# Performance work log

Measured on AMD Instinct MI355X. Metric: run time of the kernel, lower is better.

The kernel has to match this reference:

```python
import jax, jax.numpy as jnp
import numpy as np

N_EMBD = 1024
N_HEAD = 16
HEAD_DIM = N_EMBD // N_HEAD
B, T = 2, 2048


def setup_inputs() -> dict:
    key = jax.random.key(0)
    ks = jax.random.split(key, 12)
    s = 0.02
    inp = {
        "x": jax.random.normal(ks[0], (B, T, N_EMBD), dtype=jnp.float32),
        "ln1_g": jnp.ones((N_EMBD,), jnp.float32),
        "ln1_b": jnp.zeros((N_EMBD,), jnp.float32),
        "ln2_g": jnp.ones((N_EMBD,), jnp.float32),
        "ln2_b": jnp.zeros((N_EMBD,), jnp.float32),
        "W_qkv": jax.random.normal(ks[1], (N_EMBD, 3 * N_EMBD), jnp.float32) * s,
        "b_qkv": jnp.zeros((3 * N_EMBD,), jnp.float32),
        "W_o": jax.random.normal(ks[2], (N_EMBD, N_EMBD), jnp.float32) * s,
        "b_o": jnp.zeros((N_EMBD,), jnp.float32),
        "W_fc": jax.random.normal(ks[3], (N_EMBD, 4 * N_EMBD), jnp.float32) * s,
        "b_fc": jnp.zeros((4 * N_EMBD,), jnp.float32),
        "W_proj": jax.random.normal(ks[4], (4 * N_EMBD, N_EMBD), jnp.float32) * s,
        "b_proj": jnp.zeros((N_EMBD,), jnp.float32),
    }
    return inp


def _layernorm(x, g, b, eps=1e-5):
    mu = jnp.mean(x, axis=-1, keepdims=True)
    var = jnp.var(x, axis=-1, keepdims=True)
    return (x - mu) * jax.lax.rsqrt(var + eps) * g + b


def _block(x, ln1_g, ln1_b, ln2_g, ln2_b, W_qkv, b_qkv, W_o, b_o, W_fc, b_fc, W_proj, b_proj):
    # --- attention sub-block (pre-LN) ---
    h = _layernorm(x, ln1_g, ln1_b)
    qkv = h @ W_qkv + b_qkv                     # [B,T,3E]
    q, k, v = jnp.split(qkv, 3, axis=-1)
    def split_heads(t):
        return t.reshape(B, T, N_HEAD, HEAD_DIM).transpose(0, 2, 1, 3)  # [B,H,T,D]
    q, k, v = split_heads(q), split_heads(k), split_heads(v)
    scores = jnp.einsum("bhqd,bhkd->bhqk", q, k) / (HEAD_DIM ** 0.5)
    causal = jnp.tril(jnp.ones((T, T), dtype=bool))
    scores = jnp.where(causal, scores, jnp.float32(-jnp.inf))
    probs = jax.nn.softmax(scores, axis=-1)
    attn = jnp.einsum("bhqk,bhkd->bhqd", probs, v)        # [B,H,T,D]
    attn = attn.transpose(0, 2, 1, 3).reshape(B, T, N_EMBD)
    x = x + attn @ W_o + b_o
    # --- MLP sub-block (pre-LN) ---
    h = _layernorm(x, ln2_g, ln2_b)
    h = jax.nn.gelu(h @ W_fc + b_fc, approximate=False)
    x = x + h @ W_proj + b_proj
    return x


def reference(x, ln1_g, ln1_b, ln2_g, ln2_b, W_qkv, b_qkv, W_o, b_o, W_fc, b_fc, W_proj, b_proj):
    return _block(x, ln1_g, ln1_b, ln2_g, ln2_b, W_qkv, b_qkv, W_o, b_o, W_fc, b_fc, W_proj, b_proj)
```

## Files before the change

kernel.cpp:

```cpp
#include <hip/hip_runtime.h>
#include <hip/hip_bf16.h>


#define TT 2048
#define EE 1024
#define NH 16
#define HD 64

#define AS1 __attribute__((address_space(1)))
#define AS3 __attribute__((address_space(3)))

using bf16x8 = __bf16 __attribute__((ext_vector_type(8)));
using bf16x4 = __bf16 __attribute__((ext_vector_type(4)));
using f32x4  = float __attribute__((ext_vector_type(4)));

__global__ __launch_bounds__(256) void convt_kernel(const float* __restrict__ W,
                                                    __bf16* __restrict__ WT,
                                                    int K, int N) {
    __shared__ __bf16 t[32][33];
    int n0 = blockIdx.x * 32, k0 = blockIdx.y * 32;
    int tid = threadIdx.x;
    int r = tid >> 3, c4 = (tid & 7) * 4;
    float4 v = *(const float4*)(W + (size_t)(k0 + r) * N + n0 + c4);
    t[r][c4 + 0] = (__bf16)v.x; t[r][c4 + 1] = (__bf16)v.y;
    t[r][c4 + 2] = (__bf16)v.z; t[r][c4 + 3] = (__bf16)v.w;
    __syncthreads();
    bf16x4 o;
    o[0] = t[c4 + 0][r]; o[1] = t[c4 + 1][r];
    o[2] = t[c4 + 2][r]; o[3] = t[c4 + 3][r];
    *(bf16x4*)(WT + (size_t)(n0 + r) * K + k0 + c4) = o;
}

__global__ __launch_bounds__(256) void ln_kernel(const float* __restrict__ x,
                                                 const float* __restrict__ g,
                                                 const float* __restrict__ bta,
                                                 __bf16* __restrict__ out) {
    int row = blockIdx.x;
    int tid = threadIdx.x;
    const float4 xv = *(const float4*)(x + (size_t)row * EE + tid * 4);
    float s  = xv.x + xv.y + xv.z + xv.w;
    float ss = xv.x*xv.x + xv.y*xv.y + xv.z*xv.z + xv.w*xv.w;
    __shared__ float rs[256], rss[256];
    rs[tid] = s; rss[tid] = ss;
    __syncthreads();
    for (int st = 128; st > 0; st >>= 1) {
        if (tid < st) { rs[tid] += rs[tid+st]; rss[tid] += rss[tid+st]; }
        __syncthreads();
    }
    float mean = rs[0] * (1.0f / EE);
    float var  = rss[0] * (1.0f / EE) - mean * mean;
    float rstd = rsqrtf(var + 1e-5f);
    const float4 gv = *(const float4*)(g + tid * 4);
    const float4 bv = *(const float4*)(bta + tid * 4);
    bf16x4 ov;
    ov[0] = (__bf16)((xv.x - mean) * rstd * gv.x + bv.x);
    ov[1] = (__bf16)((xv.y - mean) * rstd * gv.y + bv.y);
    ov[2] = (__bf16)((xv.z - mean) * rstd * gv.z + bv.z);
    ov[3] = (__bf16)((xv.w - mean) * rstd * gv.w + bv.w);
    *(bf16x4*)(out + (size_t)row * EE + tid * 4) = ov;
}

template<int TM, int TN, bool GELU, bool RESID, typename CT>
__global__ __launch_bounds__(256) void gemm_bt_kernel(const __bf16* __restrict__ A,
                                                      const __bf16* __restrict__ BT,
                                                      const float* __restrict__ bias,
                                                      const float* resid, CT* C,
                                                      int M, int N, int K) {
    constexpr int MT = TM / 32;
    constexpr int NT = TN / 32;
    __shared__ __align__(16) __bf16 As[TM][32];
    __shared__ __align__(16) __bf16 Bs[TN][32];
    int tid = threadIdx.x, wave = tid >> 6, lane = tid & 63;
    int quad = lane >> 4, l16 = lane & 15;
    int wm = wave >> 1, wn = wave & 1;
    int m0 = blockIdx.y * TM, n0 = blockIdx.x * TN;

    f32x4 acc[MT][NT] = {};

    int srow = wave * 16 + (lane >> 2);
    int scol = (lane & 3) * 8;

    for (int kb = 0; kb < K; kb += 32) {
#pragma unroll
        for (int p = 0; p < TM / 64; p++) {
            const __bf16* g = A + (size_t)(m0 + p * 64 + srow) * K + kb + scol;
            __builtin_amdgcn_global_load_lds((AS1 const void*)g,
                                             (AS3 void*)&As[p * 64 + wave * 16][0], 16, 0, 0);
        }
#pragma unroll
        for (int p = 0; p < TN / 64; p++) {
            const __bf16* g = BT + (size_t)(n0 + p * 64 + srow) * K + kb + scol;
            __builtin_amdgcn_global_load_lds((AS1 const void*)g,
                                             (AS3 void*)&Bs[p * 64 + wave * 16][0], 16, 0, 0);
        }
        __syncthreads();
        bf16x8 af[MT], bfr[NT];
#pragma unroll
        for (int mt = 0; mt < MT; mt++)
            af[mt] = *(const bf16x8*)(&As[wm * (MT * 16) + mt * 16 + l16][quad * 8]);
#pragma unroll
        for (int nt = 0; nt < NT; nt++)
            bfr[nt] = *(const bf16x8*)(&Bs[wn * (NT * 16) + nt * 16 + l16][quad * 8]);
#pragma unroll
        for (int mt = 0; mt < MT; mt++)
#pragma unroll
            for (int nt = 0; nt < NT; nt++)
                acc[mt][nt] = __builtin_amdgcn_mfma_f32_16x16x32_bf16(af[mt], bfr[nt],
                                                                      acc[mt][nt], 0, 0, 0);
        __syncthreads();
    }

#pragma unroll
    for (int nt = 0; nt < NT; nt++) {
        int c = n0 + wn * (NT * 16) + nt * 16 + l16;
        float bv = bias[c];
#pragma unroll
        for (int mt = 0; mt < MT; mt++) {
#pragma unroll
            for (int r = 0; r < 4; r++) {
                int row = m0 + wm * (MT * 16) + mt * 16 + quad * 4 + r;
                float v = acc[mt][nt][r] + bv;
                if (GELU)  v = 0.5f * v * (1.0f + erff(v * 0.70710678118f));
                if (RESID) v += resid[(size_t)row * N + c];
                C[(size_t)row * N + c] = (CT)v;
            }
        }
    }
}

__global__ __launch_bounds__(256) void flash_attn_kernel(const __bf16* __restrict__ qkv,
                                                         __bf16* __restrict__ out) {
    int qt = (int)gridDim.x - 1 - (int)blockIdx.x;
    int h = blockIdx.y, b = blockIdx.z;
    int tid = threadIdx.x, wave = tid >> 6, lane = tid & 63;
    int quad = lane >> 4, l16 = lane & 15;
    int q0 = qt * 64;

    __shared__ __align__(16) __bf16 Ks[64][72];
    __shared__ __align__(16) __bf16 VTs[64][72];
    __shared__ __align__(16) __bf16 Ps[4][16][72];

    size_t base = (size_t)b * TT * (3 * EE);

    int qrow = q0 + wave * 16 + l16;
    const __bf16* qp = qkv + base + (size_t)qrow * (3 * EE) + h * HD;
    bf16x8 aq0 = *(const bf16x8*)(qp + quad * 8);
    bf16x8 aq1 = *(const bf16x8*)(qp + 32 + quad * 8);

    f32x4 oacc[4] = {};
    float m_i[4], l_i[4];
#pragma unroll
    for (int r = 0; r < 4; r++) { m_i[r] = -3.0e38f; l_i[r] = 0.0f; }
    int qg_base = q0 + wave * 16 + quad * 4;

    for (int kt = 0; kt <= qt; ++kt) {
        int k0 = kt * 64;
        int v = tid;
#pragma unroll
        for (int it = 0; it < 2; ++it, v += 256) {
            int row = v >> 3, col = (v & 7) * 8;
            const __bf16* kp = qkv + base + (size_t)(k0 + row) * (3 * EE) + EE + h * HD + col;
            const __bf16* vp = qkv + base + (size_t)(k0 + row) * (3 * EE) + 2 * EE + h * HD + col;
            *(bf16x8*)(&Ks[row][col]) = *(const bf16x8*)kp;
            bf16x8 vv = *(const bf16x8*)vp;
#pragma unroll
            for (int j = 0; j < 8; j++) VTs[col + j][row] = vv[j];
        }
        __syncthreads();

        f32x4 s[4] = {};
#pragma unroll
        for (int nt = 0; nt < 4; nt++) {
            bf16x8 bk0 = *(const bf16x8*)(&Ks[nt * 16 + l16][quad * 8]);
            bf16x8 bk1 = *(const bf16x8*)(&Ks[nt * 16 + l16][32 + quad * 8]);
            s[nt] = __builtin_amdgcn_mfma_f32_16x16x32_bf16(aq0, bk0, s[nt], 0, 0, 0);
            s[nt] = __builtin_amdgcn_mfma_f32_16x16x32_bf16(aq1, bk1, s[nt], 0, 0, 0);
        }

        bool maskt = (kt == qt);
        float rmax[4];
#pragma unroll
        for (int r = 0; r < 4; r++) rmax[r] = -3.0e38f;
#pragma unroll
        for (int nt = 0; nt < 4; nt++) {
            int key = k0 + nt * 16 + l16;
#pragma unroll
            for (int r = 0; r < 4; r++) {
                float sv = s[nt][r] * 0.125f;
                if (maskt && key > qg_base + r) sv = -3.0e38f;
                s[nt][r] = sv;
                rmax[r] = fmaxf(rmax[r], sv);
            }
        }
#pragma unroll
        for (int off = 1; off < 16; off <<= 1)
#pragma unroll
            for (int r = 0; r < 4; r++) rmax[r] = fmaxf(rmax[r], __shfl_xor(rmax[r], off));

        float alpha[4], rsum[4];
#pragma unroll
        for (int r = 0; r < 4; r++) {
            float mnew = fmaxf(m_i[r], rmax[r]);
            alpha[r] = __expf(m_i[r] - mnew);
            m_i[r] = mnew;
            rsum[r] = 0.0f;
        }
#pragma unroll
        for (int nt = 0; nt < 4; nt++) {
#pragma unroll
            for (int r = 0; r < 4; r++) {
                float p = __expf(s[nt][r] - m_i[r]);
                rsum[r] += p;
                Ps[wave][quad * 4 + r][nt * 16 + l16] = (__bf16)p;
            }
        }
#pragma unroll
        for (int off = 1; off < 16; off <<= 1)
#pragma unroll
            for (int r = 0; r < 4; r++) rsum[r] += __shfl_xor(rsum[r], off);
#pragma unroll
        for (int r = 0; r < 4; r++) {
            l_i[r] = l_i[r] * alpha[r] + rsum[r];
#pragma unroll
            for (int nt = 0; nt < 4; nt++) oacc[nt][r] *= alpha[r];
        }

#pragma unroll
        for (int half = 0; half < 2; half++) {
            bf16x8 ap = *(const bf16x8*)(&Ps[wave][l16][half * 32 + quad * 8]);
#pragma unroll
            for (int nt = 0; nt < 4; nt++) {
                bf16x8 bv = *(const bf16x8*)(&VTs[nt * 16 + l16][half * 32 + quad * 8]);
                oacc[nt] = __builtin_amdgcn_mfma_f32_16x16x32_bf16(ap, bv, oacc[nt], 0, 0, 0);
            }
        }
        __syncthreads();
    }

#pragma unroll
    for (int nt = 0; nt < 4; nt++) {
#pragma unroll
        for (int r = 0; r < 4; r++) {
            int qg = qg_base + r;
            out[((size_t)b * TT + qg) * EE + h * HD + nt * 16 + l16] =
                (__bf16)(oacc[nt][r] / l_i[r]);
        }
    }
}

extern "C" void kernel_launch(void* const* d_in, const int* in_sizes, int n_in,
                              void* d_out, int out_size, void* d_ws, size_t ws_size,
                              hipStream_t stream) {
    const float* x     = (const float*)d_in[0];
    const float* ln1g  = (const float*)d_in[1];
    const float* ln1b  = (const float*)d_in[2];
    const float* ln2g  = (const float*)d_in[3];
    const float* ln2b  = (const float*)d_in[4];
    const float* Wqkv  = (const float*)d_in[5];
    const float* bqkv  = (const float*)d_in[6];
    const float* Wo    = (const float*)d_in[7];
    const float* bo    = (const float*)d_in[8];
    const float* Wfc   = (const float*)d_in[9];
    const float* bfc   = (const float*)d_in[10];
    const float* Wproj = (const float*)d_in[11];
    const float* bproj = (const float*)d_in[12];
    float* out = (float*)d_out;

    const int M = 2 * TT;

    __bf16* ws = (__bf16*)d_ws;
    __bf16* regQ   = ws;
    __bf16* regS   = ws + 16777216;
    __bf16* WfcT   = ws + 20971520;
    __bf16* qkv    = regQ;
    __bf16* ff     = regQ;
    __bf16* WqkvT  = regQ + 12582912;
    __bf16* WoT    = regQ + 15728640;
    __bf16* h1 = regS, *atn = regS, *h2 = regS;
    __bf16* WprojT = regS;
    float*  x1 = out;

    convt_kernel<<<dim3(3 * EE / 32, EE / 32), 256, 0, stream>>>(Wqkv, WqkvT, EE, 3 * EE);
    convt_kernel<<<dim3(EE / 32, EE / 32), 256, 0, stream>>>(Wo, WoT, EE, EE);
    convt_kernel<<<dim3(4 * EE / 32, EE / 32), 256, 0, stream>>>(Wfc, WfcT, EE, 4 * EE);

    ln_kernel<<<M, 256, 0, stream>>>(x, ln1g, ln1b, h1);
    gemm_bt_kernel<128, 128, false, false, __bf16>
        <<<dim3(3 * EE / 128, M / 128), 256, 0, stream>>>(
        h1, WqkvT, bqkv, nullptr, qkv, M, 3 * EE, EE);
    flash_attn_kernel<<<dim3(TT / 64, NH, 2), 256, 0, stream>>>(qkv, atn);
    gemm_bt_kernel<128, 64, false, true, float>
        <<<dim3(EE / 64, M / 128), 256, 0, stream>>>(
        atn, WoT, bo, x, x1, M, EE, EE);
    ln_kernel<<<M, 256, 0, stream>>>(x1, ln2g, ln2b, h2);
    gemm_bt_kernel<128, 128, true, false, __bf16>
        <<<dim3(4 * EE / 128, M / 128), 256, 0, stream>>>(
        h2, WfcT, bfc, nullptr, ff, M, 4 * EE, EE);
    convt_kernel<<<dim3(EE / 32, 4 * EE / 32), 256, 0, stream>>>(Wproj, WprojT, 4 * EE, EE);
    gemm_bt_kernel<128, 64, false, true, float>
        <<<dim3(EE / 64, M / 128), 256, 0, stream>>>(
        ff, WprojT, bproj, x1, out, M, EE, 4 * EE);
}
```

Before: 517.1 us.

## Prefetch next K/V tile into registers and swizzle transposed V in LDS

The attention kernel now loads the next K/V tile into registers while the current tile is being computed, which overlaps global memory latency with the MFMA and softmax work. The transposed V tile in shared memory uses an XOR swizzle on the key column, so the scattered transpose writes hit different banks, and the PV reads apply the matching swizzle. This costs extra registers per thread, which could lower occupancy.

```diff
diff --git a/kernel.cpp b/kernel.cpp
--- a/kernel.cpp
+++ b/kernel.cpp
@@ -147,26 +147,42 @@
     bf16x8 aq0 = *(const bf16x8*)(qp + quad * 8);
     bf16x8 aq1 = *(const bf16x8*)(qp + 32 + quad * 8);
 
+    int srow = tid >> 3;
+    int scol = (tid & 7) * 8;
+    int r1 = srow + 32;
+    int kp0 = (srow & 7) | ((((srow >> 3) ^ (scol >> 3)) & 7) << 3);
+    int kp1 = (r1 & 7)   | ((((r1 >> 3)   ^ (scol >> 3)) & 7) << 3);
+    const __bf16* kbase = qkv + base + EE     + h * HD + scol;
+    const __bf16* vbase = qkv + base + 2 * EE + h * HD + scol;
+
     f32x4 oacc[4] = {};
     float m_i[4], l_i[4];
 #pragma unroll
     for (int r = 0; r < 4; r++) { m_i[r] = -3.0e38f; l_i[r] = 0.0f; }
     int qg_base = q0 + wave * 16 + quad * 4;
 
+    bf16x8 kr0 = *(const bf16x8*)(kbase + (size_t)srow * (3 * EE));
+    bf16x8 kr1 = *(const bf16x8*)(kbase + (size_t)r1   * (3 * EE));
+    bf16x8 vr0 = *(const bf16x8*)(vbase + (size_t)srow * (3 * EE));
+    bf16x8 vr1 = *(const bf16x8*)(vbase + (size_t)r1   * (3 * EE));
+
     for (int kt = 0; kt <= qt; ++kt) {
         int k0 = kt * 64;
-        int v = tid;
-#pragma unroll
-        for (int it = 0; it < 2; ++it, v += 256) {
-            int row = v >> 3, col = (v & 7) * 8;
-            const __bf16* kp = qkv + base + (size_t)(k0 + row) * (3 * EE) + EE + h * HD + col;
-            const __bf16* vp = qkv + base + (size_t)(k0 + row) * (3 * EE) + 2 * EE + h * HD + col;
-            *(bf16x8*)(&Ks[row][col]) = *(const bf16x8*)kp;
-            bf16x8 vv = *(const bf16x8*)vp;
-#pragma unroll
-            for (int j = 0; j < 8; j++) VTs[col + j][row] = vv[j];
-        }
-        __syncthreads();
+        *(bf16x8*)(&Ks[srow][scol]) = kr0;
+        *(bf16x8*)(&Ks[r1][scol])   = kr1;
+#pragma unroll
+        for (int j = 0; j < 8; j++) VTs[scol + j][kp0] = vr0[j];
+#pragma unroll
+        for (int j = 0; j < 8; j++) VTs[scol + j][kp1] = vr1[j];
+        __syncthreads();
+
+        if (kt < qt) {
+            size_t off = (size_t)(k0 + 64) * (3 * EE);
+            kr0 = *(const bf16x8*)(kbase + off + (size_t)srow * (3 * EE));
+            kr1 = *(const bf16x8*)(kbase + off + (size_t)r1   * (3 * EE));
+            vr0 = *(const bf16x8*)(vbase + off + (size_t)srow * (3 * EE));
+            vr1 = *(const bf16x8*)(vbase + off + (size_t)r1   * (3 * EE));
+        }
 
         f32x4 s[4] = {};
 #pragma unroll
@@ -230,7 +246,9 @@
             bf16x8 ap = *(const bf16x8*)(&Ps[wave][l16][half * 32 + quad * 8]);
 #pragma unroll
             for (int nt = 0; nt < 4; nt++) {
-                bf16x8 bv = *(const bf16x8*)(&VTs[nt * 16 + l16][half * 32 + quad * 8]);
+                int g = (nt * 2 + (l16 >> 3)) & 7;
+                int colr = (((half << 2) | quad) ^ g) << 3;
+                bf16x8 bv = *(const bf16x8*)(&VTs[nt * 16 + l16][colr]);
                 oacc[nt] = __builtin_amdgcn_mfma_f32_16x16x32_bf16(ap, bv, oacc[nt], 0, 0, 0);
             }
         }
```

Measured after the change: 475.1 us. 1.09x faster.

## Use 128-key tiles with register prefetch and swizzled V^T in flash attention

Applied to the files above, without the earlier changes.

The flash attention loop now processes 128 keys per iteration instead of 64, which halves the number of iterations and barriers. The next K/V tile is prefetched into registers while the current tile is being computed, so global loads overlap the MFMA and softmax work. The transposed V tile uses an XOR-swizzled column layout to cut LDS bank conflicts on the scattered transpose stores. The P buffer is aliased onto the K buffer to save LDS, which costs an extra barrier. The larger tile also means more wasted masked work on the diagonal tile, and higher register pressure from the prefetch registers and the eight score accumulators.

```diff
diff --git a/kernel.cpp b/kernel.cpp
--- a/kernel.cpp
+++ b/kernel.cpp
@@ -136,9 +136,8 @@
     int quad = lane >> 4, l16 = lane & 15;
     int q0 = qt * 64;
 
-    __shared__ __align__(16) __bf16 Ks[64][72];
-    __shared__ __align__(16) __bf16 VTs[64][72];
-    __shared__ __align__(16) __bf16 Ps[4][16][72];
+    __shared__ __align__(16) __bf16 KsBuf[128 * 72];
+    __shared__ __align__(16) __bf16 VTs[64][136];
 
     size_t base = (size_t)b * TT * (3 * EE);
 
@@ -147,42 +146,70 @@
     bf16x8 aq0 = *(const bf16x8*)(qp + quad * 8);
     bf16x8 aq1 = *(const bf16x8*)(qp + 32 + quad * 8);
 
+    int srow = tid >> 3;
+    int g    = tid & 7;
+    int scol = g * 8;
+    const __bf16* kbase = qkv + base + EE     + h * HD + scol;
+    const __bf16* vbase = qkv + base + 2 * EE + h * HD + scol;
+
+    __bf16* Psw = KsBuf + wave * (32 * 72);
+
     f32x4 oacc[4] = {};
     float m_i[4], l_i[4];
 #pragma unroll
     for (int r = 0; r < 4; r++) { m_i[r] = -3.0e38f; l_i[r] = 0.0f; }
     int qg_base = q0 + wave * 16 + quad * 4;
 
-    for (int kt = 0; kt <= qt; ++kt) {
-        int k0 = kt * 64;
-        int v = tid;
-#pragma unroll
-        for (int it = 0; it < 2; ++it, v += 256) {
-            int row = v >> 3, col = (v & 7) * 8;
-            const __bf16* kp = qkv + base + (size_t)(k0 + row) * (3 * EE) + EE + h * HD + col;
-            const __bf16* vp = qkv + base + (size_t)(k0 + row) * (3 * EE) + 2 * EE + h * HD + col;
-            *(bf16x8*)(&Ks[row][col]) = *(const bf16x8*)kp;
-            bf16x8 vv = *(const bf16x8*)vp;
-#pragma unroll
-            for (int j = 0; j < 8; j++) VTs[col + j][row] = vv[j];
-        }
-        __syncthreads();
-
-        f32x4 s[4] = {};
-#pragma unroll
-        for (int nt = 0; nt < 4; nt++) {
-            bf16x8 bk0 = *(const bf16x8*)(&Ks[nt * 16 + l16][quad * 8]);
-            bf16x8 bk1 = *(const bf16x8*)(&Ks[nt * 16 + l16][32 + quad * 8]);
-            s[nt] = __builtin_amdgcn_mfma_f32_16x16x32_bf16(aq0, bk0, s[nt], 0, 0, 0);
-            s[nt] = __builtin_amdgcn_mfma_f32_16x16x32_bf16(aq1, bk1, s[nt], 0, 0, 0);
-        }
-
-        bool maskt = (kt == qt);
+    int nIter = (qt >> 1) + 1;
+
+    bf16x8 kr[4], vr[4];
+#pragma unroll
+    for (int p = 0; p < 4; p++) {
+        kr[p] = *(const bf16x8*)(kbase + (size_t)(32 * p + srow) * (3 * EE));
+        vr[p] = *(const bf16x8*)(vbase + (size_t)(32 * p + srow) * (3 * EE));
+    }
+
+    for (int kt = 0; kt < nIter; ++kt) {
+        int k0 = kt * 128;
+#pragma unroll
+        for (int p = 0; p < 4; p++) {
+            int key = 32 * p + srow;
+            *(bf16x8*)(&KsBuf[key * 72 + scol]) = kr[p];
+            int kb = key >> 3, k7 = key & 7;
+#pragma unroll
+            for (int j = 0; j < 8; j++) {
+                int pc = ((kb ^ (g ^ j)) << 3) | k7;
+                VTs[scol + j][pc] = vr[p][j];
+            }
+        }
+        __syncthreads();
+
+        if (kt < nIter - 1) {
+            int kn = k0 + 128;
+#pragma unroll
+            for (int p = 0; p < 4; p++) {
+                kr[p] = *(const bf16x8*)(kbase + (size_t)(kn + 32 * p + srow) * (3 * EE));
+                vr[p] = *(const bf16x8*)(vbase + (size_t)(kn + 32 * p + srow) * (3 * EE));
+            }
+        }
+
+        f32x4 s[8];
+#pragma unroll
+        for (int nt = 0; nt < 8; nt++) {
+            bf16x8 bk0 = *(const bf16x8*)(&KsBuf[(nt * 16 + l16) * 72 + quad * 8]);
+            bf16x8 bk1 = *(const bf16x8*)(&KsBuf[(nt * 16 + l16) * 72 + 32 + quad * 8]);
+            f32x4 z = {};
+            z = __builtin_amdgcn_mfma_f32_16x16x32_bf16(aq0, bk0, z, 0, 0, 0);
+            s[nt] = __builtin_amdgcn_mfma_f32_16x16x32_bf16(aq1, bk1, z, 0, 0, 0);
+        }
+        __syncthreads();
+
+        bool maskt = (kt == nIter - 1);
         float rmax[4];
 #pragma unroll
         for (int r = 0; r < 4; r++) rmax[r] = -3.0e38f;
 #pragma unroll
-        for (int nt = 0; nt < 4; nt++) {
+        for (int nt = 0; nt < 8; nt++) {
             int key = k0 + nt * 16 + l16;
 #pragma unroll
             for (int r = 0; r < 4; r++) {
@@ -206,12 +233,12 @@
             rsum[r] = 0.0f;
         }
 #pragma unroll
-        for (int nt = 0; nt < 4; nt++) {
+        for (int nt = 0; nt < 8; nt++) {
 #pragma unroll
             for (int r = 0; r < 4; r++) {
                 float p = __expf(s[nt][r] - m_i[r]);
                 rsum[r] += p;
-                Ps[wave][quad * 4 + r][nt * 16 + l16] = (__bf16)p;
+                Psw[(quad * 4 + r) * 136 + nt * 16 + l16] = (__bf16)p;
             }
         }
 #pragma unroll
@@ -222,28 +249,30 @@
         for (int r = 0; r < 4; r++) {
             l_i[r] = l_i[r] * alpha[r] + rsum[r];
 #pragma unroll
-            for (int nt = 0; nt < 4; nt++) oacc[nt][r] *= alpha[r];
-        }
-
-#pragma unroll
-        for (int half = 0; half < 2; half++) {
-            bf16x8 ap = *(const bf16x8*)(&Ps[wave][l16][half * 32 + quad * 8]);
-#pragma unroll
-            for (int nt = 0; nt < 4; nt++) {
-                bf16x8 bv = *(const bf16x8*)(&VTs[nt * 16 + l16][half * 32 + quad * 8]);
-                oacc[nt] = __builtin_amdgcn_mfma_f32_16x16x32_bf16(ap, bv, oacc[nt], 0, 0, 0);
-            }
-        }
-        __syncthreads();
-    }
-
-#pragma unroll
-    for (int nt = 0; nt < 4; nt++) {
+            for (int dt = 0; dt < 4; dt++) oacc[dt][r] *= alpha[r];
+        }
+
+#pragma unroll
+        for (int w = 0; w < 4; w++) {
+            bf16x8 ap = *(const bf16x8*)(&Psw[l16 * 136 + w * 32 + quad * 8]);
+#pragma unroll
+            for (int dt = 0; dt < 4; dt++) {
+                int fd = ((2 * dt + (l16 >> 3)) ^ l16) & 7;
+                int cb = (4 * w + quad) ^ fd;
+                bf16x8 bv = *(const bf16x8*)(&VTs[dt * 16 + l16][cb * 8]);
+                oacc[dt] = __builtin_amdgcn_mfma_f32_16x16x32_bf16(ap, bv, oacc[dt], 0, 0, 0);
+            }
+        }
+        __syncthreads();
+    }
+
+#pragma unroll
+    for (int dt = 0; dt < 4; dt++) {
 #pragma unroll
         for (int r = 0; r < 4; r++) {
             int qg = qg_base + r;
-            out[((size_t)b * TT + qg) * EE + h * HD + nt * 16 + l16] =
-                (__bf16)(oacc[nt][r] / l_i[r]);
+            out[((size_t)b * TT + qg) * EE + h * HD + dt * 16 + l16] =
+                (__bf16)(oacc[dt][r] / l_i[r]);
         }
     }
 }
```

Result: faster. 470.7 us (-9.0%).
